# Kernel optimization log

Hardware: AMD Instinct MI355X
Metric: run time of the kernel (lower is better)

Reference implementation:

```python
import jax, jax.numpy as jnp
import numpy as np

L = 512       # seq_len (capped by hard-coded max_length=512)
LEN = 2048    # input feature dim ('length')
D = 2048      # d_model
H = 16        # num_heads
DH = D // H   # d_head = 128
FF = 8192     # FFN hidden
EPS = 1e-5


def _pos_encoding(n, d):
    # Matches PositionalEncoderLayer buffer construction exactly.
    pos = jnp.arange(n, dtype=jnp.float32)[:, None]                              # [n,1]
    freqs = 1.0 / (2.0 * jnp.pi) / (10000.0 * jnp.exp(jnp.arange(0, d, 2, dtype=jnp.float32) / d))
    pe = jnp.zeros((n, d), dtype=jnp.float32)
    pe = pe.at[:, 0::2].set(jnp.sin(2.0 * jnp.pi * freqs * pos))
    pe = pe.at[:, 1::2].set(jnp.cos(2.0 * jnp.pi * freqs * pos))
    return pe


def _layernorm(x, g, b):
    mu = jnp.mean(x, axis=-1, keepdims=True)
    var = jnp.mean((x - mu) ** 2, axis=-1, keepdims=True)
    return (x - mu) / jnp.sqrt(var + EPS) * g + b


def setup_inputs() -> dict:
    key = jax.random.key(0)
    ks = jax.random.split(key, 12)
    def lin(k, fin, fout):
        kw, kb = jax.random.split(k)
        W = jax.random.normal(kw, (fin, fout), jnp.float32) / np.sqrt(fin)
        b = jax.random.normal(kb, (fout,), jnp.float32) * 0.01
        return W, b
    emb_W, emb_b = lin(ks[0], LEN, D)
    Wq, bq = lin(ks[1], D, D)
    Wk, bk = lin(ks[2], D, D)
    Wv, bv = lin(ks[3], D, D)
    Wo, bo = lin(ks[4], D, D)
    W1, b1 = lin(ks[5], D, FF)
    W2, b2 = lin(ks[6], FF, D)
    return {
        "sequence": jax.random.normal(ks[7], (L, LEN), jnp.float32),
        "emb_W": emb_W, "emb_b": emb_b,
        "Wq": Wq, "bq": bq, "Wk": Wk, "bk": bk, "Wv": Wv, "bv": bv,
        "Wo": Wo, "bo": bo,
        "ln_g": jnp.ones((D,), jnp.float32), "ln_b": jnp.zeros((D,), jnp.float32),
        "W1": W1, "b1": b1, "W2": W2, "b2": b2,
    }


def reference(sequence, emb_W, emb_b, Wq, bq, Wk, bk, Wv, bv, Wo, bo, ln_g, ln_b, W1, b1, W2, b2):
    # Embedding + positional encoding
    X = sequence @ emb_W + emb_b                         # [L, D]
    X = X + _pos_encoding(X.shape[0], X.shape[1])
    # Multi-head attention (keeps the module's [L, d_head, H] layout)
    Q = (X @ Wq + bq).reshape(-1, DH, H)
    K = (X @ Wk + bk).reshape(-1, DH, H)
    V = (X @ Wv + bv).reshape(-1, DH, H)
    scores = jnp.einsum('ldh,mdh->lmh', Q, K) / jnp.sqrt(jnp.float32(D))  # [L, L, H]
    attn = jax.nn.softmax(scores, axis=1)                # softmax over keys
    A = jnp.einsum('lmh,mdh->ldh', attn, V).reshape(-1, D) @ Wo + bo
    # Residual + shared LayerNorm, FFN, residual + shared LayerNorm
    Xa = _layernorm(A + X, ln_g, ln_b)
    F = jax.nn.gelu(Xa @ W1 + b1) @ W2 + b2
    return _layernorm(F + Xa, ln_g, ln_b)
```

## Files before the change

kernel.cpp:

```cpp
#include <hip/hip_runtime.h>
#include <hip/hip_bf16.h>


typedef __bf16 bf16_t;
typedef __bf16 bf16x4 __attribute__((ext_vector_type(4)));
typedef __bf16 bf16x8 __attribute__((ext_vector_type(8)));
typedef float  f32x4  __attribute__((ext_vector_type(4)));

#define SEQL 512
#define DM   2048
#define FFH  8192
#define NH   16
#define DHD  128
#define PST  ((size_t)SEQL*DM)

__device__ __forceinline__ unsigned short bfbits(float f){
  bf16_t h = (bf16_t)f;
  return __builtin_bit_cast(unsigned short, h);
}
__device__ __forceinline__ unsigned int pack2(float a, float b){
  return (unsigned int)bfbits(a) | ((unsigned int)bfbits(b) << 16);
}

__device__ __forceinline__ void gll16(const bf16_t* g, bf16_t* l){
  __builtin_amdgcn_global_load_lds(
      (const __attribute__((address_space(1))) void*)g,
      (__attribute__((address_space(3))) void*)l, 16, 0, 0);
}
__device__ __forceinline__ unsigned lds_off(const void* p){
  return (unsigned)(uintptr_t)(const __attribute__((address_space(3))) void*)p;
}

struct CvtSeg { const float* src; bf16_t* dst; int base; };
struct CvtArgs { CvtSeg s[8]; };

__global__ __launch_bounds__(256)
void cvt_all(CvtArgs a){
  const int b = blockIdx.x;
  int i = 0;
#pragma unroll
  for (int j = 1; j < 8; ++j) if (b >= a.s[j].base) i = j;
  const size_t off = ((size_t)(b - a.s[i].base) * 2048) + threadIdx.x * 8;
  const float4 v0 = *(const float4*)(a.s[i].src + off);
  const float4 v1 = *(const float4*)(a.s[i].src + off + 4);
  uint4 o;
  o.x = pack2(v0.x, v0.y); o.y = pack2(v0.z, v0.w);
  o.z = pack2(v1.x, v1.y); o.w = pack2(v1.z, v1.w);
  *(uint4*)(a.s[i].dst + off) = o;
}

constexpr int E_PART = 0;
constexpr int E_QKV  = 1;
constexpr int E_FFN1 = 2;

template<int EPI, int PERM, int BM>
__global__ __launch_bounds__(256, (BM == 64) ? 3 : 4)
void gemmT(const bf16_t* __restrict__ A,
           const bf16_t* __restrict__ B0, const bf16_t* __restrict__ B1,
           const bf16_t* __restrict__ B2,
           const float* __restrict__ b0p, const float* __restrict__ b1p,
           const float* __restrict__ b2p,
           float* __restrict__ outF, bf16_t* __restrict__ o0,
           bf16_t* __restrict__ o1, bf16_t* __restrict__ o2,
           int nn, int Nw, int K, int Kc)
{
  constexpr int NF    = (BM == 64) ? 4 : 2;
  constexpr int APASS = BM / 32;
  constexpr int MTM   = (BM == 64) ? 7 : 15;
  constexpr int MTS   = (BM == 64) ? 3 : 4;
  __shared__ bf16_t sA[2][BM*64];
  __shared__ bf16_t sB[2][128*64];
  const int tid  = threadIdx.x;
  const int lane = tid & 63, w = tid >> 6;
  const int wr4 = (BM == 64) ? (w >> 1) : 0;
  const int wc  = (BM == 64) ? (w & 1)  : w;
  const int c = lane & 15, g = lane >> 4;

  const int nwg = gridDim.x, cpx = nwg >> 3;
  const int sblk = (blockIdx.x & 7) * cpx + (blockIdx.x >> 3);
  const int mt = sblk & MTM, q2 = sblk >> MTS;
  const int nt = q2 % nn, zt = q2 / nn;
  const int m0 = mt * BM, k0 = zt * Kc;

  const bf16_t* Bsel = B0; int nb0 = nt * 128;
  if constexpr (EPI == E_QKV){
    if (nt >= 32){ Bsel = B2; nb0 = (nt - 32) * 128; }
    else if (nt >= 16){ Bsel = B1; nb0 = (nt - 16) * 128; }
  }

  const int arow = tid >> 3;
  const int acol = (((tid & 7) ^ ((tid >> 3) & 7)) << 3);
  const bf16_t* Aps[APASS];
#pragma unroll
  for (int pa = 0; pa < APASS; ++pa)
    Aps[pa] = A + (size_t)(m0 + pa*32 + arow) * K + k0 + acol;

  const int klB  = (lane >> 3) * 4 + ((lane >> 1) & 3);
  const int colB = nb0 + w*16 + (lane & 1)*8;
  const bf16_t* Bph[2];
  if constexpr (!PERM){
#pragma unroll
    for (int h = 0; h < 2; ++h)
      Bph[h] = Bsel + (size_t)(k0 + h*32 + klB) * Nw + colB;
  }

  const unsigned sBbase[2] = { lds_off(&sB[0][0]), lds_off(&sB[1][0]) };
  const unsigned trLane = (unsigned)(g*256 + c*8);

  f32x4 acc[2][NF] = {};
  const int nk = Kc >> 6;

#define STAGE(bf, kt) {                                                     \
    _Pragma("unroll")                                                       \
    for (int pa = 0; pa < APASS; ++pa)                                      \
      gll16(Aps[pa] + (size_t)(kt)*64, &sA[bf][(pa*256 + tid)*8]);          \
    _Pragma("unroll")                                                       \
    for (int h = 0; h < 2; ++h)                                             \
      _Pragma("unroll")                                                     \
      for (int p = 0; p < 2; ++p){                                          \
        const bf16_t* src;                                                  \
        if constexpr (PERM){                                                \
          const int kr = k0 + (kt)*64 + h*32 + klB;                         \
          const int krow = ((kr & 127) << 4) + (kr >> 7);                   \
          src = Bsel + (size_t)krow * Nw + colB + p*64;                     \
        } else {                                                            \
          src = Bph[h] + (size_t)(kt)*64*Nw + p*64;                         \
        }                                                                   \
        gll16(src, &sB[bf][h*4096 + (p*256 + tid)*8]);                      \
      } }

#define COMPUTE(PB) {                                                       \
    bf16x8 af[2][2]; bf16x8 bq[NF][2];                                      \
    _Pragma("unroll")                                                       \
    for (int m = 0; m < 2; ++m)                                             \
      _Pragma("unroll")                                                     \
      for (int ks = 0; ks < 2; ++ks){                                       \
        const int r = wr4*32 + m*16 + c;                                    \
        af[m][ks] = *(const bf16x8*)&sA[PB][r*64 + (((ks*4+g) ^ (r&7))<<3)];\
      }                                                                     \
    { const unsigned base = sBbase[PB] + (unsigned)(wc*NF*1024) + trLane;   \
      _Pragma("unroll")                                                     \
      for (int n = 0; n < NF; ++n)                                          \
        _Pragma("unroll")                                                   \
        for (int ks = 0; ks < 2; ++ks){                                     \
          bf16x4 r0, r1;                                                    \
          const unsigned a2 = base + (unsigned)(n*1024 + ks*8192);          \
          asm volatile("ds_read_b64_tr_b16 %0, %1" : "=v"(r0) : "v"(a2));   \
          asm volatile("ds_read_b64_tr_b16 %0, %1 offset:128" : "=v"(r1) : "v"(a2)); \
          bq[n][ks] = __builtin_shufflevector(r0, r1, 0,1,2,3,4,5,6,7);     \
        } }                                                                 \
    asm volatile("s_waitcnt lgkmcnt(0)" ::: "memory");                      \
    __builtin_amdgcn_sched_barrier(0);                                      \
    _Pragma("unroll")                                                       \
    for (int m = 0; m < 2; ++m)                                             \
      _Pragma("unroll")                                                     \
      for (int n = 0; n < NF; ++n)                                          \
        _Pragma("unroll")                                                   \
        for (int ks = 0; ks < 2; ++ks)                                      \
          acc[m][n] = __builtin_amdgcn_mfma_f32_16x16x32_bf16(af[m][ks], bq[n][ks], acc[m][n], 0,0,0); }

  STAGE(0, 0);
  asm volatile("s_waitcnt vmcnt(0)" ::: "memory");
  __builtin_amdgcn_s_barrier();
  __builtin_amdgcn_sched_barrier(0);

  int buf = 0;
  for (int kt = 0; kt < nk; ++kt){
    if (kt + 1 < nk){ STAGE(buf ^ 1, kt + 1); }
    COMPUTE(buf);
    asm volatile("s_waitcnt vmcnt(0)" ::: "memory");
    __builtin_amdgcn_s_barrier();
    __builtin_amdgcn_sched_barrier(0);
    buf ^= 1;
  }
#undef STAGE
#undef COMPUTE

#pragma unroll
  for (int n = 0; n < NF; ++n){
    const int col = nt*128 + wc*(NF*16) + n*16 + c;
#pragma unroll
    for (int m = 0; m < 2; ++m){
      const int row0 = m0 + wr4*32 + m*16 + 4*g;
      const f32x4 a4 = acc[m][n];
      if constexpr (EPI == E_PART){
        float* dst = outF + (size_t)zt * PST;
#pragma unroll
        for (int rr = 0; rr < 4; ++rr)
          dst[(size_t)(row0+rr)*DM + col] = a4[rr];
      } else if constexpr (EPI == E_QKV){
        if (col < DM){
          const float bv = b0p[col];
#pragma unroll
          for (int rr = 0; rr < 4; ++rr)
            o0[(size_t)(row0+rr)*DM + col] = (bf16_t)(a4[rr] + bv);
        } else if (col < 2*DM){
          const int cc = col - DM;
          const float bv = b1p[cc];
#pragma unroll
          for (int rr = 0; rr < 4; ++rr)
            o1[(size_t)(row0+rr)*DM + cc] = (bf16_t)(a4[rr] + bv);
        } else {
          const int cc = col - 2*DM;
          const float bv = b2p[cc];
          const int hh = cc & 15, dd = cc >> 4;
          unsigned short us[4];
#pragma unroll
          for (int rr = 0; rr < 4; ++rr) us[rr] = bfbits(a4[rr] + bv);
          *(ushort4*)&o2[(size_t)(hh*DHD + dd)*SEQL + row0] =
              make_ushort4(us[0], us[1], us[2], us[3]);
        }
      } else if constexpr (EPI == E_FFN1){
        const float bv = b0p[col];
#pragma unroll
        for (int rr = 0; rr < 4; ++rr){
          const float v = a4[rr] + bv;
          const float z = v * (v*v*0.044715f + 1.0f) * 1.5957691216f;
          const float gg = v / (1.0f + __expf(-z));
          o0[(size_t)(row0+rr)*FFH + col] = (bf16_t)gg;
        }
      }
    }
  }
}

__global__ __launch_bounds__(256)
void permute_qk(const bf16_t* __restrict__ Qf, const bf16_t* __restrict__ Kf,
                bf16_t* __restrict__ Qhd, bf16_t* __restrict__ Khd)
{
  const int row = blockIdx.x, which = blockIdx.y, tid = threadIdx.x;
  const bf16_t* src = (which ? Kf : Qf) + (size_t)row * DM;
  bf16_t* dst = which ? Khd : Qhd;
  const int hh = tid >> 4, d0 = (tid & 15) * 8;
  unsigned short us[8];
#pragma unroll
  for (int j = 0; j < 8; ++j)
    us[j] = __builtin_bit_cast(unsigned short, src[(d0 + j)*NH + hh]);
  uint4 o;
  o.x = (unsigned)us[0] | ((unsigned)us[1] << 16);
  o.y = (unsigned)us[2] | ((unsigned)us[3] << 16);
  o.z = (unsigned)us[4] | ((unsigned)us[5] << 16);
  o.w = (unsigned)us[6] | ((unsigned)us[7] << 16);
  *(uint4*)&dst[(size_t)hh*(SEQL*DHD) + (size_t)row*DHD + d0] = o;
}

__global__ __launch_bounds__(256)
void attn_kernel(const bf16_t* __restrict__ Qh, const bf16_t* __restrict__ Kh,
                 const bf16_t* __restrict__ Vt, bf16_t* __restrict__ Aout)
{
  __shared__ bf16_t Pl[32*512];
  __shared__ float redm[4][32];
  __shared__ float reds[4][32];
  const int tid = threadIdx.x;
  const int lane = tid & 63, w = tid >> 6;
  const int c = lane & 15, g = lane >> 4;
  const int h = blockIdx.y;
  const int rb = blockIdx.x * 32;
  const bf16_t* Qb = Qh + (size_t)h * (SEQL*DHD);
  const bf16_t* Kb = Kh + (size_t)h * (SEQL*DHD);
  const bf16_t* Vb = Vt + (size_t)h * (SEQL*DHD);

  bf16x8 qf[2][4];
#pragma unroll
  for (int a = 0; a < 2; ++a)
#pragma unroll
    for (int ks = 0; ks < 4; ++ks)
      qf[a][ks] = *(const bf16x8*)(Qb + (size_t)(rb + a*16 + c)*DHD + ks*32 + g*8);

  f32x4 s[2][8] = {};
#pragma unroll
  for (int ks = 0; ks < 4; ++ks)
#pragma unroll
    for (int b = 0; b < 8; ++b){
      const bf16x8 kf = *(const bf16x8*)(Kb + (size_t)(w*128 + b*16 + c)*DHD + ks*32 + g*8);
      s[0][b] = __builtin_amdgcn_mfma_f32_16x16x32_bf16(qf[0][ks], kf, s[0][b], 0,0,0);
      s[1][b] = __builtin_amdgcn_mfma_f32_16x16x32_bf16(qf[1][ks], kf, s[1][b], 0,0,0);
    }
#pragma unroll
  for (int a = 0; a < 2; ++a)
#pragma unroll
    for (int b = 0; b < 8; ++b)
#pragma unroll
      for (int rr = 0; rr < 4; ++rr) s[a][b][rr] *= 0.022097086912079612f;

  float mx[2][4], sm[2][4], inv[2][4];
#pragma unroll
  for (int a = 0; a < 2; ++a)
#pragma unroll
    for (int rr = 0; rr < 4; ++rr){
      float m = s[a][0][rr];
#pragma unroll
      for (int b = 1; b < 8; ++b) m = fmaxf(m, s[a][b][rr]);
#pragma unroll
      for (int off = 1; off < 16; off <<= 1) m = fmaxf(m, __shfl_xor(m, off));
      mx[a][rr] = m;
    }
  if (c == 0)
#pragma unroll
    for (int a = 0; a < 2; ++a)
#pragma unroll
      for (int rr = 0; rr < 4; ++rr) redm[w][a*16 + 4*g + rr] = mx[a][rr];
  __syncthreads();
#pragma unroll
  for (int a = 0; a < 2; ++a)
#pragma unroll
    for (int rr = 0; rr < 4; ++rr){
      const int lr = a*16 + 4*g + rr;
      mx[a][rr] = fmaxf(fmaxf(redm[0][lr], redm[1][lr]), fmaxf(redm[2][lr], redm[3][lr]));
      sm[a][rr] = 0.f;
    }
#pragma unroll
  for (int a = 0; a < 2; ++a)
#pragma unroll
    for (int b = 0; b < 8; ++b)
#pragma unroll
      for (int rr = 0; rr < 4; ++rr){
        const float p = __expf(s[a][b][rr] - mx[a][rr]);
        s[a][b][rr] = p;
        sm[a][rr] += p;
      }
#pragma unroll
  for (int a = 0; a < 2; ++a)
#pragma unroll
    for (int rr = 0; rr < 4; ++rr){
#pragma unroll
      for (int off = 1; off < 16; off <<= 1) sm[a][rr] += __shfl_xor(sm[a][rr], off);
    }
  if (c == 0)
#pragma unroll
    for (int a = 0; a < 2; ++a)
#pragma unroll
      for (int rr = 0; rr < 4; ++rr) reds[w][a*16 + 4*g + rr] = sm[a][rr];
  __syncthreads();
#pragma unroll
  for (int a = 0; a < 2; ++a)
#pragma unroll
    for (int rr = 0; rr < 4; ++rr){
      const int lr = a*16 + 4*g + rr;
      inv[a][rr] = 1.0f / (reds[0][lr] + reds[1][lr] + reds[2][lr] + reds[3][lr]);
    }

#pragma unroll
  for (int a = 0; a < 2; ++a)
#pragma unroll
    for (int b = 0; b < 8; ++b)
#pragma unroll
      for (int rr = 0; rr < 4; ++rr){
        const int lr  = a*16 + 4*g + rr;
        const int key = w*128 + b*16 + c;
        const int slot = (key >> 3) ^ (lr & 7);
        Pl[lr*512 + slot*8 + (key & 7)] = (bf16_t)(s[a][b][rr] * inv[a][rr]);
      }
  __syncthreads();

  f32x4 o[2][2] = {};
  const int dw = w * 32;
#pragma unroll
  for (int kst = 0; kst < 16; ++kst){
    bf16x8 pa2[2];
#pragma unroll
    for (int a = 0; a < 2; ++a){
      const int r = a*16 + c;
      const int slot = (kst*4 + g) ^ (r & 7);
      pa2[a] = *(const bf16x8*)&Pl[r*512 + slot*8];
    }
#pragma unroll
    for (int db = 0; db < 2; ++db){
      const bf16x8 vf = *(const bf16x8*)(Vb + (size_t)(dw + db*16 + c)*SEQL + kst*32 + g*8);
      o[0][db] = __builtin_amdgcn_mfma_f32_16x16x32_bf16(pa2[0], vf, o[0][db], 0,0,0);
      o[1][db] = __builtin_amdgcn_mfma_f32_16x16x32_bf16(pa2[1], vf, o[1][db], 0,0,0);
    }
  }
#pragma unroll
  for (int a = 0; a < 2; ++a)
#pragma unroll
    for (int db = 0; db < 2; ++db)
#pragma unroll
      for (int rr = 0; rr < 4; ++rr){
        const int row  = rb + a*16 + 4*g + rr;
        const int col2 = h*DHD + dw + db*16 + c;
        Aout[(size_t)row*DM + col2] = (bf16_t)o[a][db][rr];
      }
}

template<int S>
__global__ __launch_bounds__(256)
void reduce_pos(const float* __restrict__ P, const float* __restrict__ bias,
                float* __restrict__ X, bf16_t* __restrict__ XB)
{
  const int row = blockIdx.x, c0 = threadIdx.x * 8;
  const size_t base = (size_t)row * DM + c0;
  float y[8];
#pragma unroll
  for (int j = 0; j < 8; ++j) y[j] = bias[c0 + j];
#pragma unroll
  for (int s = 0; s < S; ++s){
    const float4 v0 = *(const float4*)(P + s*PST + base);
    const float4 v1 = *(const float4*)(P + s*PST + base + 4);
    y[0]+=v0.x; y[1]+=v0.y; y[2]+=v0.z; y[3]+=v0.w;
    y[4]+=v1.x; y[5]+=v1.y; y[6]+=v1.z; y[7]+=v1.w;
  }
#pragma unroll
  for (int j = 0; j < 8; ++j){
    const int col = c0 + j;
    const float fr  = 1e-4f * __expf(-(float)(col >> 1) * (1.0f/1024.0f));
    const float ang = (float)row * fr;
    y[j] += (col & 1) ? __cosf(ang) : __sinf(ang);
  }
  *(float4*)(X + base)     = make_float4(y[0], y[1], y[2], y[3]);
  *(float4*)(X + base + 4) = make_float4(y[4], y[5], y[6], y[7]);
  uint4 ob;
  ob.x = pack2(y[0], y[1]); ob.y = pack2(y[2], y[3]);
  ob.z = pack2(y[4], y[5]); ob.w = pack2(y[6], y[7]);
  *(uint4*)&XB[base] = ob;
}

template<int S, int WB>
__global__ __launch_bounds__(256)
void reduce_ln(const float* __restrict__ P, const float* __restrict__ bias,
               const float* __restrict__ resid, const float* __restrict__ gam,
               const float* __restrict__ bet, float* __restrict__ outF,
               bf16_t* __restrict__ outB)
{
  const int row = blockIdx.x, tid = threadIdx.x, c0 = tid * 8;
  const size_t base = (size_t)row * DM + c0;
  float y[8];
  {
    const float4 r0 = *(const float4*)(resid + base);
    const float4 r1 = *(const float4*)(resid + base + 4);
    y[0]=r0.x; y[1]=r0.y; y[2]=r0.z; y[3]=r0.w;
    y[4]=r1.x; y[5]=r1.y; y[6]=r1.z; y[7]=r1.w;
  }
#pragma unroll
  for (int j = 0; j < 8; ++j) y[j] += bias[c0 + j];
#pragma unroll
  for (int s = 0; s < S; ++s){
    const float4 v0 = *(const float4*)(P + s*PST + base);
    const float4 v1 = *(const float4*)(P + s*PST + base + 4);
    y[0]+=v0.x; y[1]+=v0.y; y[2]+=v0.z; y[3]+=v0.w;
    y[4]+=v1.x; y[5]+=v1.y; y[6]+=v1.z; y[7]+=v1.w;
  }
  float sm = 0.f, qs = 0.f;
#pragma unroll
  for (int j = 0; j < 8; ++j){ sm += y[j]; qs += y[j]*y[j]; }
#pragma unroll
  for (int off = 32; off >= 1; off >>= 1){
    sm += __shfl_xor(sm, off); qs += __shfl_xor(qs, off);
  }
  __shared__ float rs[4], rq[4];
  const int w = tid >> 6;
  if ((tid & 63) == 0){ rs[w] = sm; rq[w] = qs; }
  __syncthreads();
  sm = rs[0]+rs[1]+rs[2]+rs[3];
  qs = rq[0]+rq[1]+rq[2]+rq[3];
  const float mu   = sm * (1.0f/2048.0f);
  const float var  = qs * (1.0f/2048.0f) - mu*mu;
  const float rstd = rsqrtf(var + 1e-5f);
  const float4 g0 = *(const float4*)(gam + c0);
  const float4 g1 = *(const float4*)(gam + c0 + 4);
  const float4 b0 = *(const float4*)(bet + c0);
  const float4 b1 = *(const float4*)(bet + c0 + 4);
  float o[8];
  o[0] = (y[0]-mu)*rstd*g0.x + b0.x;  o[1] = (y[1]-mu)*rstd*g0.y + b0.y;
  o[2] = (y[2]-mu)*rstd*g0.z + b0.z;  o[3] = (y[3]-mu)*rstd*g0.w + b0.w;
  o[4] = (y[4]-mu)*rstd*g1.x + b1.x;  o[5] = (y[5]-mu)*rstd*g1.y + b1.y;
  o[6] = (y[6]-mu)*rstd*g1.z + b1.z;  o[7] = (y[7]-mu)*rstd*g1.w + b1.w;
  *(float4*)(outF + base)     = make_float4(o[0], o[1], o[2], o[3]);
  *(float4*)(outF + base + 4) = make_float4(o[4], o[5], o[6], o[7]);
  if constexpr (WB){
    uint4 ob;
    ob.x = pack2(o[0], o[1]); ob.y = pack2(o[2], o[3]);
    ob.z = pack2(o[4], o[5]); ob.w = pack2(o[6], o[7]);
    *(uint4*)&outB[base] = ob;
  }
}

extern "C" void kernel_launch(void* const* d_in, const int* in_sizes, int n_in,
                              void* d_out, int out_size, void* d_ws, size_t ws_size,
                              hipStream_t stream)
{
  const float* seq   = (const float*)d_in[0];
  const float* emb_W = (const float*)d_in[1];
  const float* emb_b = (const float*)d_in[2];
  const float* Wq = (const float*)d_in[3];  const float* bq = (const float*)d_in[4];
  const float* Wk = (const float*)d_in[5];  const float* bk = (const float*)d_in[6];
  const float* Wv = (const float*)d_in[7];  const float* bv = (const float*)d_in[8];
  const float* Wo = (const float*)d_in[9];  const float* bo = (const float*)d_in[10];
  const float* ln_g = (const float*)d_in[11]; const float* ln_b = (const float*)d_in[12];
  const float* W1 = (const float*)d_in[13]; const float* b1 = (const float*)d_in[14];
  const float* W2 = (const float*)d_in[15]; const float* b2 = (const float*)d_in[16];

  char* ws = (char*)d_ws;
  size_t off = 0;
  auto take = [&](size_t bytes) -> void* {
    void* p = ws + off;
    off += (bytes + 255) & ~(size_t)255;
    return p;
  };
  bf16_t* seqB = (bf16_t*)take((size_t)SEQL*DM*2);
  bf16_t* WeB  = (bf16_t*)take((size_t)DM*DM*2);
  bf16_t* WqB  = (bf16_t*)take((size_t)DM*DM*2);
  bf16_t* WkB  = (bf16_t*)take((size_t)DM*DM*2);
  bf16_t* WvB  = (bf16_t*)take((size_t)DM*DM*2);
  bf16_t* WoB  = (bf16_t*)take((size_t)DM*DM*2);
  bf16_t* W1B  = (bf16_t*)take((size_t)DM*FFH*2);
  bf16_t* W2B  = (bf16_t*)take((size_t)FFH*DM*2);
  float*  X    = (float*) take((size_t)SEQL*DM*4);
  bf16_t* XB   = (bf16_t*)take((size_t)SEQL*DM*2);
  bf16_t* Qf   = (bf16_t*)take((size_t)SEQL*DM*2);
  bf16_t* Kf   = (bf16_t*)take((size_t)SEQL*DM*2);
  bf16_t* Qhd  = (bf16_t*)take((size_t)SEQL*DM*2);
  bf16_t* Khd  = (bf16_t*)take((size_t)SEQL*DM*2);
  bf16_t* Vt   = (bf16_t*)take((size_t)SEQL*DM*2);
  bf16_t* Afl  = (bf16_t*)take((size_t)SEQL*DM*2);
  float*  Pp   = (float*) take((size_t)8*SEQL*DM*4);
  float*  Xa   = (float*) take((size_t)SEQL*DM*4);
  bf16_t* XaB  = (bf16_t*)take((size_t)SEQL*DM*2);
  bf16_t* Hb   = (bf16_t*)take((size_t)SEQL*FFH*2);
  (void)ws_size; (void)in_sizes; (void)n_in; (void)out_size;

  CvtArgs ca;
  ca.s[0] = { seq,   seqB,     0 };
  ca.s[1] = { emb_W, WeB,    512 };
  ca.s[2] = { Wq,    WqB,   2560 };
  ca.s[3] = { Wk,    WkB,   4608 };
  ca.s[4] = { Wv,    WvB,   6656 };
  ca.s[5] = { Wo,    WoB,   8704 };
  ca.s[6] = { W1,    W1B,  10752 };
  ca.s[7] = { W2,    W2B,  18944 };
  cvt_all<<<dim3(27136), 256, 0, stream>>>(ca);

  gemmT<E_PART,0,64><<<dim3(512), 256, 0, stream>>>(seqB, WeB, nullptr, nullptr,
      nullptr, nullptr, nullptr, Pp, nullptr, nullptr, nullptr, 16, DM, DM, 512);
  reduce_pos<4><<<SEQL, 256, 0, stream>>>(Pp, emb_b, X, XB);

  gemmT<E_QKV,0,32><<<dim3(768), 256, 0, stream>>>(XB, WqB, WkB, WvB,
      bq, bk, bv, nullptr, Qf, Kf, Vt, 48, DM, DM, DM);
  permute_qk<<<dim3(SEQL,2), 256, 0, stream>>>(Qf, Kf, Qhd, Khd);

  attn_kernel<<<dim3(16,16), 256, 0, stream>>>(Qhd, Khd, Vt, Afl);

  gemmT<E_PART,1,64><<<dim3(512), 256, 0, stream>>>(Afl, WoB, nullptr, nullptr,
      nullptr, nullptr, nullptr, Pp, nullptr, nullptr, nullptr, 16, DM, DM, 512);
  reduce_ln<4,1><<<SEQL, 256, 0, stream>>>(Pp, bo, X, ln_g, ln_b, Xa, XaB);

  gemmT<E_FFN1,0,32><<<dim3(1024), 256, 0, stream>>>(XaB, W1B, nullptr, nullptr,
      b1, nullptr, nullptr, nullptr, Hb, nullptr, nullptr, 64, FFH, DM, DM);

  gemmT<E_PART,0,64><<<dim3(1024), 256, 0, stream>>>(Hb, W2B, nullptr, nullptr,
      nullptr, nullptr, nullptr, Pp, nullptr, nullptr, nullptr, 16, DM, FFH, 1024);
  reduce_ln<8,0><<<SEQL, 256, 0, stream>>>(Pp, b2, Xa, ln_g, ln_b, (float*)d_out, nullptr);
}
```

Baseline: 239.0 us.

## Fuse weight fp32-to-bf16 conversion blocks into earlier GEMM and attention launches

The single upfront conversion kernel is split up. Only the sequence and embedding weight are converted first. The Wq/Wk/Wv, W1 and Wo/W2 conversions are appended as extra blocks to the embedding GEMM, the QKV GEMM and the attention kernel, so that memory-bound conversion overlaps with compute-bound stages that run before those weights are needed. Each conversion block now handles 8K elements instead of 2K. The catch is larger grids with mixed block types, which may affect occupancy and scheduling of the GEMM blocks.

```diff
diff --git a/kernel.cpp b/kernel.cpp
--- a/kernel.cpp
+++ b/kernel.cpp
@@ -32,28 +32,42 @@
 }
 
 struct CvtSeg { const float* src; bf16_t* dst; int base; };
-struct CvtArgs { CvtSeg s[8]; };
-
+struct CvtA3  { CvtSeg s[3]; };
+
+template<int NS>
+__device__ __forceinline__ void cvt_block8k(const CvtSeg* segs, int b){
+  int i = 0;
+#pragma unroll
+  for (int j = 1; j < NS; ++j) if (b >= segs[j].base) i = j;
+  const float* src = segs[i].src;
+  bf16_t* dst = segs[i].dst;
+  const size_t off0 = (size_t)(b - segs[i].base) * 8192 + threadIdx.x * 8;
+  f32x4 v[8];
+#pragma unroll
+  for (int it = 0; it < 4; ++it){
+    v[2*it]   = *(const f32x4*)(src + off0 + it*2048);
+    v[2*it+1] = *(const f32x4*)(src + off0 + it*2048 + 4);
+  }
+#pragma unroll
+  for (int it = 0; it < 4; ++it){
+    uint4 o;
+    o.x = pack2(v[2*it][0],   v[2*it][1]);
+    o.y = pack2(v[2*it][2],   v[2*it][3]);
+    o.z = pack2(v[2*it+1][0], v[2*it+1][1]);
+    o.w = pack2(v[2*it+1][2], v[2*it+1][3]);
+    *(uint4*)(dst + off0 + it*2048) = o;
+  }
+}
+
+template<int NS>
 __global__ __launch_bounds__(256)
-void cvt_all(CvtArgs a){
-  const int b = blockIdx.x;
-  int i = 0;
-#pragma unroll
-  for (int j = 1; j < 8; ++j) if (b >= a.s[j].base) i = j;
-  const size_t off = ((size_t)(b - a.s[i].base) * 2048) + threadIdx.x * 8;
-  const float4 v0 = *(const float4*)(a.s[i].src + off);
-  const float4 v1 = *(const float4*)(a.s[i].src + off + 4);
-  uint4 o;
-  o.x = pack2(v0.x, v0.y); o.y = pack2(v0.z, v0.w);
-  o.z = pack2(v1.x, v1.y); o.w = pack2(v1.z, v1.w);
-  *(uint4*)(a.s[i].dst + off) = o;
-}
+void cvt8k(CvtA3 a){ cvt_block8k<NS>(a.s, blockIdx.x); }
 
 constexpr int E_PART = 0;
 constexpr int E_QKV  = 1;
 constexpr int E_FFN1 = 2;
 
-template<int EPI, int PERM, int BM>
+template<int EPI, int PERM, int BM, int NCVT>
 __global__ __launch_bounds__(256, (BM == 64) ? 3 : 4)
 void gemmT(const bf16_t* __restrict__ A,
            const bf16_t* __restrict__ B0, const bf16_t* __restrict__ B1,
@@ -62,8 +76,14 @@
            const float* __restrict__ b2p,
            float* __restrict__ outF, bf16_t* __restrict__ o0,
            bf16_t* __restrict__ o1, bf16_t* __restrict__ o2,
-           int nn, int Nw, int K, int Kc)
+           int nn, int Nw, int K, int Kc, int gemmN, CvtA3 cva)
 {
+  if constexpr (NCVT > 0){
+    if ((int)blockIdx.x >= gemmN){
+      cvt_block8k<NCVT>(cva.s, (int)blockIdx.x - gemmN);
+      return;
+    }
+  }
   constexpr int NF    = (BM == 64) ? 4 : 2;
   constexpr int APASS = BM / 32;
   constexpr int MTM   = (BM == 64) ? 7 : 15;
@@ -76,8 +96,8 @@
   const int wc  = (BM == 64) ? (w & 1)  : w;
   const int c = lane & 15, g = lane >> 4;
 
-  const int nwg = gridDim.x, cpx = nwg >> 3;
-  const int sblk = (blockIdx.x & 7) * cpx + (blockIdx.x >> 3);
+  const int cpx = gemmN >> 3;
+  const int sblk = ((int)blockIdx.x & 7) * cpx + ((int)blockIdx.x >> 3);
   const int mt = sblk & MTM, q2 = sblk >> MTS;
   const int nt = q2 % nn, zt = q2 / nn;
   const int m0 = mt * BM, k0 = zt * Kc;
@@ -244,18 +264,26 @@
   *(uint4*)&dst[(size_t)hh*(SEQL*DHD) + (size_t)row*DHD + d0] = o;
 }
 
+template<int NCVT>
 __global__ __launch_bounds__(256)
-void attn_kernel(const bf16_t* __restrict__ Qh, const bf16_t* __restrict__ Kh,
-                 const bf16_t* __restrict__ Vt, bf16_t* __restrict__ Aout)
+void attn_cvt(const bf16_t* __restrict__ Qh, const bf16_t* __restrict__ Kh,
+              const bf16_t* __restrict__ Vt, bf16_t* __restrict__ Aout,
+              int attnN, CvtA3 cva)
 {
+  if constexpr (NCVT > 0){
+    if ((int)blockIdx.x >= attnN){
+      cvt_block8k<NCVT>(cva.s, (int)blockIdx.x - attnN);
+      return;
+    }
+  }
   __shared__ bf16_t Pl[32*512];
   __shared__ float redm[4][32];
   __shared__ float reds[4][32];
   const int tid = threadIdx.x;
   const int lane = tid & 63, w = tid >> 6;
   const int c = lane & 15, g = lane >> 4;
-  const int h = blockIdx.y;
-  const int rb = blockIdx.x * 32;
+  const int h  = (int)blockIdx.x >> 4;
+  const int rb = ((int)blockIdx.x & 15) * 32;
   const bf16_t* Qb = Qh + (size_t)h * (SEQL*DHD);
   const bf16_t* Kb = Kh + (size_t)h * (SEQL*DHD);
   const bf16_t* Vb = Vt + (size_t)h * (SEQL*DHD);
@@ -519,35 +547,40 @@
   bf16_t* Hb   = (bf16_t*)take((size_t)SEQL*FFH*2);
   (void)ws_size; (void)in_sizes; (void)n_in; (void)out_size;
 
-  CvtArgs ca;
-  ca.s[0] = { seq,   seqB,     0 };
-  ca.s[1] = { emb_W, WeB,    512 };
-  ca.s[2] = { Wq,    WqB,   2560 };
-  ca.s[3] = { Wk,    WkB,   4608 };
-  ca.s[4] = { Wv,    WvB,   6656 };
-  ca.s[5] = { Wo,    WoB,   8704 };
-  ca.s[6] = { W1,    W1B,  10752 };
-  ca.s[7] = { W2,    W2B,  18944 };
-  cvt_all<<<dim3(27136), 256, 0, stream>>>(ca);
-
-  gemmT<E_PART,0,64><<<dim3(512), 256, 0, stream>>>(seqB, WeB, nullptr, nullptr,
-      nullptr, nullptr, nullptr, Pp, nullptr, nullptr, nullptr, 16, DM, DM, 512);
+  CvtA3 cz = {};
+
+  CvtA3 c0 = {};
+  c0.s[0] = { seq,   seqB, 0 };
+  c0.s[1] = { emb_W, WeB,  128 };
+  cvt8k<2><<<dim3(640), 256, 0, stream>>>(c0);
+
+  CvtA3 cq = {};
+  cq.s[0] = { Wq, WqB, 0 };
+  cq.s[1] = { Wk, WkB, 512 };
+  cq.s[2] = { Wv, WvB, 1024 };
+  gemmT<E_PART,0,64,3><<<dim3(2048), 256, 0, stream>>>(seqB, WeB, nullptr, nullptr,
+      nullptr, nullptr, nullptr, Pp, nullptr, nullptr, nullptr, 16, DM, DM, 512, 512, cq);
   reduce_pos<4><<<SEQL, 256, 0, stream>>>(Pp, emb_b, X, XB);
 
-  gemmT<E_QKV,0,32><<<dim3(768), 256, 0, stream>>>(XB, WqB, WkB, WvB,
-      bq, bk, bv, nullptr, Qf, Kf, Vt, 48, DM, DM, DM);
+  CvtA3 c1 = {};
+  c1.s[0] = { W1, W1B, 0 };
+  gemmT<E_QKV,0,32,1><<<dim3(2816), 256, 0, stream>>>(XB, WqB, WkB, WvB,
+      bq, bk, bv, nullptr, Qf, Kf, Vt, 48, DM, DM, DM, 768, c1);
   permute_qk<<<dim3(SEQL,2), 256, 0, stream>>>(Qf, Kf, Qhd, Khd);
 
-  attn_kernel<<<dim3(16,16), 256, 0, stream>>>(Qhd, Khd, Vt, Afl);
-
-  gemmT<E_PART,1,64><<<dim3(512), 256, 0, stream>>>(Afl, WoB, nullptr, nullptr,
-      nullptr, nullptr, nullptr, Pp, nullptr, nullptr, nullptr, 16, DM, DM, 512);
+  CvtA3 c2 = {};
+  c2.s[0] = { Wo, WoB, 0 };
+  c2.s[1] = { W2, W2B, 512 };
+  attn_cvt<2><<<dim3(2816), 256, 0, stream>>>(Qhd, Khd, Vt, Afl, 256, c2);
+
+  gemmT<E_PART,1,64,0><<<dim3(512), 256, 0, stream>>>(Afl, WoB, nullptr, nullptr,
+      nullptr, nullptr, nullptr, Pp, nullptr, nullptr, nullptr, 16, DM, DM, 512, 512, cz);
   reduce_ln<4,1><<<SEQL, 256, 0, stream>>>(Pp, bo, X, ln_g, ln_b, Xa, XaB);
 
-  gemmT<E_FFN1,0,32><<<dim3(1024), 256, 0, stream>>>(XaB, W1B, nullptr, nullptr,
-      b1, nullptr, nullptr, nullptr, Hb, nullptr, nullptr, 64, FFH, DM, DM);
-
-  gemmT<E_PART,0,64><<<dim3(1024), 256, 0, stream>>>(Hb, W2B, nullptr, nullptr,
-      nullptr, nullptr, nullptr, Pp, nullptr, nullptr, nullptr, 16, DM, FFH, 1024);
+  gemmT<E_FFN1,0,32,0><<<dim3(1024), 256, 0, stream>>>(XaB, W1B, nullptr, nullptr,
+      b1, nullptr, nullptr, nullptr, Hb, nullptr, nullptr, 64, FFH, DM, DM, 1024, cz);
+
+  gemmT<E_PART,0,64,0><<<dim3(1024), 256, 0, stream>>>(Hb, W2B, nullptr, nullptr,
+      nullptr, nullptr, nullptr, Pp, nullptr, nullptr, nullptr, 16, DM, FFH, 1024, 1024, cz);
   reduce_ln<8,0><<<SEQL, 256, 0, stream>>>(Pp, b2, Xa, ln_g, ln_b, (float*)d_out, nullptr);
 }
```

Result: faster. 223.5 us (-6.5%).

## Fuse fp32 weight conversion into GEMM loads via register-staged pipeline

Applied to the files above, without the earlier changes.

Removes the separate kernel that converted every fp32 weight matrix to bf16. The GEMM now reads fp32 weights straight from global memory into registers, converts them to bf16, and writes them to LDS, using a two-deep register prefetch in place of direct global-to-LDS loads. This avoids a full write and re-read of the converted weights, at the cost of twice the weight bytes per GEMM load, more register pressure (occupancy hint lowered to 2), and an extra barrier per iteration. The W2 GEMM split-K factor also drops from 8 to 4 to halve the partial-sum buffer and its reduction.

```diff
diff --git a/kernel.cpp b/kernel.cpp
--- a/kernel.cpp
+++ b/kernel.cpp
@@ -21,32 +21,28 @@
 __device__ __forceinline__ unsigned int pack2(float a, float b){
   return (unsigned int)bfbits(a) | ((unsigned int)bfbits(b) << 16);
 }
-
-__device__ __forceinline__ void gll16(const bf16_t* g, bf16_t* l){
-  __builtin_amdgcn_global_load_lds(
-      (const __attribute__((address_space(1))) void*)g,
-      (__attribute__((address_space(3))) void*)l, 16, 0, 0);
-}
 __device__ __forceinline__ unsigned lds_off(const void* p){
   return (unsigned)(uintptr_t)(const __attribute__((address_space(3))) void*)p;
 }
 
-struct CvtSeg { const float* src; bf16_t* dst; int base; };
-struct CvtArgs { CvtSeg s[8]; };
-
 __global__ __launch_bounds__(256)
-void cvt_all(CvtArgs a){
-  const int b = blockIdx.x;
-  int i = 0;
-#pragma unroll
-  for (int j = 1; j < 8; ++j) if (b >= a.s[j].base) i = j;
-  const size_t off = ((size_t)(b - a.s[i].base) * 2048) + threadIdx.x * 8;
-  const float4 v0 = *(const float4*)(a.s[i].src + off);
-  const float4 v1 = *(const float4*)(a.s[i].src + off + 4);
-  uint4 o;
-  o.x = pack2(v0.x, v0.y); o.y = pack2(v0.z, v0.w);
-  o.z = pack2(v1.x, v1.y); o.w = pack2(v1.z, v1.w);
-  *(uint4*)(a.s[i].dst + off) = o;
+void cvt_seq(const float* __restrict__ src, bf16_t* __restrict__ dst){
+  const size_t off0 = (size_t)blockIdx.x * 8192 + threadIdx.x * 8;
+  f32x4 v[8];
+#pragma unroll
+  for (int it = 0; it < 4; ++it){
+    v[2*it]   = *(const f32x4*)(src + off0 + it*2048);
+    v[2*it+1] = *(const f32x4*)(src + off0 + it*2048 + 4);
+  }
+#pragma unroll
+  for (int it = 0; it < 4; ++it){
+    uint4 u;
+    u.x = pack2(v[2*it][0],   v[2*it][1]);
+    u.y = pack2(v[2*it][2],   v[2*it][3]);
+    u.z = pack2(v[2*it+1][0], v[2*it+1][1]);
+    u.w = pack2(v[2*it+1][2], v[2*it+1][3]);
+    *(uint4*)(dst + off0 + it*2048) = u;
+  }
 }
 
 constexpr int E_PART = 0;
@@ -54,10 +50,10 @@
 constexpr int E_FFN1 = 2;
 
 template<int EPI, int PERM, int BM>
-__global__ __launch_bounds__(256, (BM == 64) ? 3 : 4)
-void gemmT(const bf16_t* __restrict__ A,
-           const bf16_t* __restrict__ B0, const bf16_t* __restrict__ B1,
-           const bf16_t* __restrict__ B2,
+__global__ __launch_bounds__(256, 2)
+void gemmF(const bf16_t* __restrict__ A,
+           const float* __restrict__ W0p, const float* __restrict__ W1p,
+           const float* __restrict__ W2p,
            const float* __restrict__ b0p, const float* __restrict__ b1p,
            const float* __restrict__ b2p,
            float* __restrict__ outF, bf16_t* __restrict__ o0,
@@ -77,15 +73,15 @@
   const int c = lane & 15, g = lane >> 4;
 
   const int nwg = gridDim.x, cpx = nwg >> 3;
-  const int sblk = (blockIdx.x & 7) * cpx + (blockIdx.x >> 3);
+  const int sblk = ((int)blockIdx.x & 7) * cpx + ((int)blockIdx.x >> 3);
   const int mt = sblk & MTM, q2 = sblk >> MTS;
   const int nt = q2 % nn, zt = q2 / nn;
   const int m0 = mt * BM, k0 = zt * Kc;
 
-  const bf16_t* Bsel = B0; int nb0 = nt * 128;
+  const float* Wp = W0p; int nb0 = nt * 128;
   if constexpr (EPI == E_QKV){
-    if (nt >= 32){ Bsel = B2; nb0 = (nt - 32) * 128; }
-    else if (nt >= 16){ Bsel = B1; nb0 = (nt - 16) * 128; }
+    if (nt >= 32){ Wp = W2p; nb0 = (nt - 32) * 128; }
+    else if (nt >= 16){ Wp = W1p; nb0 = (nt - 16) * 128; }
   }
 
   const int arow = tid >> 3;
@@ -97,12 +93,6 @@
 
   const int klB  = (lane >> 3) * 4 + ((lane >> 1) & 3);
   const int colB = nb0 + w*16 + (lane & 1)*8;
-  const bf16_t* Bph[2];
-  if constexpr (!PERM){
-#pragma unroll
-    for (int h = 0; h < 2; ++h)
-      Bph[h] = Bsel + (size_t)(k0 + h*32 + klB) * Nw + colB;
-  }
 
   const unsigned sBbase[2] = { lds_off(&sB[0][0]), lds_off(&sB[1][0]) };
   const unsigned trLane = (unsigned)(g*256 + c*8);
@@ -110,23 +100,36 @@
   f32x4 acc[2][NF] = {};
   const int nk = Kc >> 6;
 
-#define STAGE(bf, kt) {                                                     \
+#define LOADST(SA, SB, kt) {                                                \
     _Pragma("unroll")                                                       \
     for (int pa = 0; pa < APASS; ++pa)                                      \
-      gll16(Aps[pa] + (size_t)(kt)*64, &sA[bf][(pa*256 + tid)*8]);          \
+      SA[pa] = *(const uint4*)(Aps[pa] + (size_t)(kt)*64);                  \
     _Pragma("unroll")                                                       \
     for (int h = 0; h < 2; ++h)                                             \
       _Pragma("unroll")                                                     \
       for (int p = 0; p < 2; ++p){                                          \
-        const bf16_t* src;                                                  \
-        if constexpr (PERM){                                                \
-          const int kr = k0 + (kt)*64 + h*32 + klB;                         \
-          const int krow = ((kr & 127) << 4) + (kr >> 7);                   \
-          src = Bsel + (size_t)krow * Nw + colB + p*64;                     \
-        } else {                                                            \
-          src = Bph[h] + (size_t)(kt)*64*Nw + p*64;                         \
-        }                                                                   \
-        gll16(src, &sB[bf][h*4096 + (p*256 + tid)*8]);                      \
+        const int kr = k0 + (kt)*64 + h*32 + klB;                           \
+        const int krow = PERM ? (((kr & 127) << 4) + (kr >> 7)) : kr;       \
+        const float* s3 = Wp + (size_t)krow * Nw + colB + p*64;             \
+        SB[h*2+p][0] = *(const f32x4*)s3;                                   \
+        SB[h*2+p][1] = *(const f32x4*)(s3 + 4);                             \
+      }                                                                     \
+    __builtin_amdgcn_sched_barrier(0); }
+
+#define WRITEST(bf, SA, SB) {                                               \
+    _Pragma("unroll")                                                       \
+    for (int pa = 0; pa < APASS; ++pa)                                      \
+      *(uint4*)&sA[bf][(pa*256 + tid)*8] = SA[pa];                          \
+    _Pragma("unroll")                                                       \
+    for (int h = 0; h < 2; ++h)                                             \
+      _Pragma("unroll")                                                     \
+      for (int p = 0; p < 2; ++p){                                          \
+        uint4 v;                                                            \
+        v.x = pack2(SB[h*2+p][0][0], SB[h*2+p][0][1]);                      \
+        v.y = pack2(SB[h*2+p][0][2], SB[h*2+p][0][3]);                      \
+        v.z = pack2(SB[h*2+p][1][0], SB[h*2+p][1][1]);                      \
+        v.w = pack2(SB[h*2+p][1][2], SB[h*2+p][1][3]);                      \
+        *(uint4*)&sB[bf][h*4096 + (p*256 + tid)*8] = v;                     \
       } }
 
 #define COMPUTE(PB) {                                                       \
@@ -159,22 +162,36 @@
         for (int ks = 0; ks < 2; ++ks)                                      \
           acc[m][n] = __builtin_amdgcn_mfma_f32_16x16x32_bf16(af[m][ks], bq[n][ks], acc[m][n], 0,0,0); }
 
-  STAGE(0, 0);
-  asm volatile("s_waitcnt vmcnt(0)" ::: "memory");
+#define ITER(kt, PB, SLa, SLb, SCa, SCb) {                                  \
+    if ((kt) + 2 < nk) LOADST(SLa, SLb, (kt)+2);                            \
+    COMPUTE(PB);                                                            \
+    __builtin_amdgcn_s_barrier();                                           \
+    __builtin_amdgcn_sched_barrier(0);                                      \
+    if ((kt) + 1 < nk){                                                     \
+      WRITEST(PB^1, SCa, SCb);                                              \
+      asm volatile("s_waitcnt lgkmcnt(0)" ::: "memory");                    \
+      __builtin_amdgcn_s_barrier();                                         \
+      __builtin_amdgcn_sched_barrier(0);                                    \
+    } }
+
+  uint4 a0[APASS], a1[APASS];
+  f32x4 b0s[4][2], b1s[4][2];
+
+  LOADST(a0, b0s, 0);
+  LOADST(a1, b1s, 1);
+  WRITEST(0, a0, b0s);
+  asm volatile("s_waitcnt lgkmcnt(0)" ::: "memory");
   __builtin_amdgcn_s_barrier();
   __builtin_amdgcn_sched_barrier(0);
 
-  int buf = 0;
-  for (int kt = 0; kt < nk; ++kt){
-    if (kt + 1 < nk){ STAGE(buf ^ 1, kt + 1); }
-    COMPUTE(buf);
-    asm volatile("s_waitcnt vmcnt(0)" ::: "memory");
-    __builtin_amdgcn_s_barrier();
-    __builtin_amdgcn_sched_barrier(0);
-    buf ^= 1;
-  }
-#undef STAGE
+  for (int kt = 0; kt < nk; kt += 2){
+    ITER(kt,     0, a0, b0s, a1, b1s);
+    ITER(kt + 1, 1, a1, b1s, a0, b0s);
+  }
+#undef LOADST
+#undef WRITEST
 #undef COMPUTE
+#undef ITER
 
 #pragma unroll
   for (int n = 0; n < NF; ++n){
@@ -498,13 +515,6 @@
     return p;
   };
   bf16_t* seqB = (bf16_t*)take((size_t)SEQL*DM*2);
-  bf16_t* WeB  = (bf16_t*)take((size_t)DM*DM*2);
-  bf16_t* WqB  = (bf16_t*)take((size_t)DM*DM*2);
-  bf16_t* WkB  = (bf16_t*)take((size_t)DM*DM*2);
-  bf16_t* WvB  = (bf16_t*)take((size_t)DM*DM*2);
-  bf16_t* WoB  = (bf16_t*)take((size_t)DM*DM*2);
-  bf16_t* W1B  = (bf16_t*)take((size_t)DM*FFH*2);
-  bf16_t* W2B  = (bf16_t*)take((size_t)FFH*DM*2);
   float*  X    = (float*) take((size_t)SEQL*DM*4);
   bf16_t* XB   = (bf16_t*)take((size_t)SEQL*DM*2);
   bf16_t* Qf   = (bf16_t*)take((size_t)SEQL*DM*2);
@@ -513,41 +523,32 @@
   bf16_t* Khd  = (bf16_t*)take((size_t)SEQL*DM*2);
   bf16_t* Vt   = (bf16_t*)take((size_t)SEQL*DM*2);
   bf16_t* Afl  = (bf16_t*)take((size_t)SEQL*DM*2);
-  float*  Pp   = (float*) take((size_t)8*SEQL*DM*4);
+  float*  Pp   = (float*) take((size_t)4*SEQL*DM*4);
   float*  Xa   = (float*) take((size_t)SEQL*DM*4);
   bf16_t* XaB  = (bf16_t*)take((size_t)SEQL*DM*2);
   bf16_t* Hb   = (bf16_t*)take((size_t)SEQL*FFH*2);
   (void)ws_size; (void)in_sizes; (void)n_in; (void)out_size;
 
-  CvtArgs ca;
-  ca.s[0] = { seq,   seqB,     0 };
-  ca.s[1] = { emb_W, WeB,    512 };
-  ca.s[2] = { Wq,    WqB,   2560 };
-  ca.s[3] = { Wk,    WkB,   4608 };
-  ca.s[4] = { Wv,    WvB,   6656 };
-  ca.s[5] = { Wo,    WoB,   8704 };
-  ca.s[6] = { W1,    W1B,  10752 };
-  ca.s[7] = { W2,    W2B,  18944 };
-  cvt_all<<<dim3(27136), 256, 0, stream>>>(ca);
-
-  gemmT<E_PART,0,64><<<dim3(512), 256, 0, stream>>>(seqB, WeB, nullptr, nullptr,
+  cvt_seq<<<dim3(128), 256, 0, stream>>>(seq, seqB);
+
+  gemmF<E_PART,0,64><<<dim3(512), 256, 0, stream>>>(seqB, emb_W, nullptr, nullptr,
       nullptr, nullptr, nullptr, Pp, nullptr, nullptr, nullptr, 16, DM, DM, 512);
   reduce_pos<4><<<SEQL, 256, 0, stream>>>(Pp, emb_b, X, XB);
 
-  gemmT<E_QKV,0,32><<<dim3(768), 256, 0, stream>>>(XB, WqB, WkB, WvB,
+  gemmF<E_QKV,0,32><<<dim3(768), 256, 0, stream>>>(XB, Wq, Wk, Wv,
       bq, bk, bv, nullptr, Qf, Kf, Vt, 48, DM, DM, DM);
   permute_qk<<<dim3(SEQL,2), 256, 0, stream>>>(Qf, Kf, Qhd, Khd);
 
   attn_kernel<<<dim3(16,16), 256, 0, stream>>>(Qhd, Khd, Vt, Afl);
 
-  gemmT<E_PART,1,64><<<dim3(512), 256, 0, stream>>>(Afl, WoB, nullptr, nullptr,
+  gemmF<E_PART,1,64><<<dim3(512), 256, 0, stream>>>(Afl, Wo, nullptr, nullptr,
       nullptr, nullptr, nullptr, Pp, nullptr, nullptr, nullptr, 16, DM, DM, 512);
   reduce_ln<4,1><<<SEQL, 256, 0, stream>>>(Pp, bo, X, ln_g, ln_b, Xa, XaB);
 
-  gemmT<E_FFN1,0,32><<<dim3(1024), 256, 0, stream>>>(XaB, W1B, nullptr, nullptr,
+  gemmF<E_FFN1,0,32><<<dim3(1024), 256, 0, stream>>>(XaB, W1, nullptr, nullptr,
       b1, nullptr, nullptr, nullptr, Hb, nullptr, nullptr, 64, FFH, DM, DM);
 
-  gemmT<E_PART,0,64><<<dim3(1024), 256, 0, stream>>>(Hb, W2B, nullptr, nullptr,
-      nullptr, nullptr, nullptr, Pp, nullptr, nullptr, nullptr, 16, DM, FFH, 1024);
-  reduce_ln<8,0><<<SEQL, 256, 0, stream>>>(Pp, b2, Xa, ln_g, ln_b, (float*)d_out, nullptr);
-}
+  gemmF<E_PART,0,64><<<dim3(512), 256, 0, stream>>>(Hb, W2, nullptr, nullptr,
+      nullptr, nullptr, nullptr, Pp, nullptr, nullptr, nullptr, 16, DM, FFH, 2048);
+  reduce_ln<4,0><<<SEQL, 256, 0, stream>>>(Pp, b2, Xa, ln_g, ln_b, (float*)d_out, nullptr);
+}
```

After: 352.4 us. 47.4% more time.
